# Performance work log

Measured on AMD Instinct MI355X. Metric: run time of the kernel, lower is better.

The kernel has to match this reference:

```python
import jax, jax.numpy as jnp
import numpy as np
import math

N_EMB = 768
N_HEAD = 12
N_INNER = 3072
B, T = 2, 2048
EPS = 1e-4


def _gelu_tanh(x):
    return x * 0.5 * (1.0 + jnp.tanh(math.sqrt(2.0 / math.pi) * (x + 0.044715 * x ** 3)))


def _layernorm(x, scale, bias):
    mean = jnp.mean(x, axis=-1, keepdims=True)
    var = jnp.var(x, axis=-1, keepdims=True, ddof=1)  # torch.var default: unbiased
    return scale * ((x - mean) / jnp.sqrt(var + EPS)) + bias


def setup_inputs() -> dict:
    key = jax.random.key(0)
    ks = jax.random.split(key, 16)
    s_attn = 1.0 / math.sqrt(N_EMB)
    s_mlp1 = 1.0 / math.sqrt(N_EMB)
    s_mlp2 = 1.0 / math.sqrt(N_INNER)
    return {
        "x": jax.random.normal(ks[0], (B, T, N_EMB), dtype=jnp.float32),
        "Wq": jax.random.normal(ks[1], (N_EMB, N_EMB), dtype=jnp.float32) * s_attn,
        "bq": jnp.zeros((N_EMB,), jnp.float32),
        "Wk": jax.random.normal(ks[2], (N_EMB, N_EMB), dtype=jnp.float32) * s_attn,
        "bk": jnp.zeros((N_EMB,), jnp.float32),
        "Wv": jax.random.normal(ks[3], (N_EMB, N_EMB), dtype=jnp.float32) * s_attn,
        "bv": jnp.zeros((N_EMB,), jnp.float32),
        "Wo": jax.random.normal(ks[4], (N_EMB, N_EMB), dtype=jnp.float32) * s_attn,
        "bo": jnp.zeros((N_EMB,), jnp.float32),
        "ln1_s": jnp.ones((N_EMB,), jnp.float32),
        "ln1_b": jnp.zeros((N_EMB,), jnp.float32),
        "W1": jax.random.normal(ks[5], (N_EMB, N_INNER), dtype=jnp.float32) * s_mlp1,
        "b1": jnp.zeros((N_INNER,), jnp.float32),
        "W2": jax.random.normal(ks[6], (N_INNER, N_EMB), dtype=jnp.float32) * s_mlp2,
        "b2": jnp.zeros((N_EMB,), jnp.float32),
        "ln2_s": jnp.ones((N_EMB,), jnp.float32),
        "ln2_b": jnp.zeros((N_EMB,), jnp.float32),
    }


def reference(x, Wq, bq, Wk, bk, Wv, bv, Wo, bo, ln1_s, ln1_b, W1, b1, W2, b2, ln2_s, ln2_b):
    Bx, Tx, C = x.shape
    dh = C // N_HEAD
    # QKV projections -> [B, H, T, dh]
    def split_heads(y):
        return y.reshape(Bx, Tx, N_HEAD, dh).transpose(0, 2, 1, 3)
    q = split_heads(x @ Wq + bq)
    k = split_heads(x @ Wk + bk)
    v = split_heads(x @ Wv + bv)
    # naive full-score causal attention (materializes [B,H,T,T])
    scores = jnp.einsum("bhqd,bhkd->bhqk", q, k)
    causal = jnp.tril(jnp.ones((Tx, Tx), dtype=bool))
    scores = jnp.where(causal, scores, -jnp.inf)
    attn = jax.nn.softmax(scores / math.sqrt(dh), axis=-1)
    ctx = jnp.einsum("bhqk,bhkd->bhqd", attn, v)
    ctx = ctx.transpose(0, 2, 1, 3).reshape(Bx, Tx, C)
    attn_out = ctx @ Wo + bo
    # post-norm residual
    h = _layernorm(x + attn_out, ln1_s, ln1_b)
    mlp_out = _gelu_tanh(h @ W1 + b1) @ W2 + b2
    return _layernorm(h + mlp_out, ln2_s, ln2_b)
```

## Files before the change

kernel.cpp:

```cpp
#include <hip/hip_runtime.h>
#include <math.h>

#define TB  2
#define TT  2048
#define TC  768
#define TH  12
#define TDH 64
#define TI  3072
#define TM  (TB*TT)

typedef __attribute__((ext_vector_type(8))) __bf16 bf16x8;
typedef __attribute__((ext_vector_type(4))) __bf16 bf16x4;
typedef __attribute__((ext_vector_type(4))) float  f32x4;

__device__ __forceinline__ float gelu_tanh(float x) {
    float x3 = x * x * x;
    return 0.5f * x * (1.0f + tanhf(0.7978845608028654f * (x + 0.044715f * x3)));
}

__device__ __forceinline__ void gld_lds16(const void* g, void* l) {
    __builtin_amdgcn_global_load_lds(
        (const __attribute__((address_space(1))) unsigned int*)g,
        (__attribute__((address_space(3))) unsigned int*)l,
        16, 0, 0);
}

#define BK 32

template<int BM_, int BN_, int WM_, int WN_>
__global__ __launch_bounds__(256)
void gemm_mfma(const __bf16* __restrict__ A, const __bf16* __restrict__ Bt,
               const float* __restrict__ b0, const float* __restrict__ b1,
               const float* __restrict__ b2, const float* __restrict__ resid,
               float* __restrict__ outf, __bf16* __restrict__ outb,
               int N, int K, size_t wt_stride, size_t out_stride, int ep)
{
    constexpr int WAVES_N = BN_ / WN_;
    constexpr int TMt = WM_ / 16, TNt = WN_ / 16;
    constexpr int AISS = BM_ / 64, BISS = BN_ / 64;
    constexpr int TILE = (BM_ + BN_) * BK;
    __shared__ __align__(16) __bf16 lds[2 * TILE];

    const int tid  = threadIdx.x;
    const int wave = tid >> 6, lane = tid & 63;
    const int wm = wave / WAVES_N, wn = wave % WAVES_N;
    const int m0 = blockIdx.y * BM_, n0 = blockIdx.x * BN_;
    const int z  = blockIdx.z;

    const __bf16* Bz = Bt + (size_t)z * wt_stride;
    const size_t Kb = (size_t)K * 2;
    const char* Ag = (const char*)A + (size_t)m0 * Kb;
    const char* Bg = (const char*)Bz + (size_t)n0 * Kb;
    const int srow = tid >> 2;
    const int scol = ((tid & 3) ^ ((tid >> 4) & 3)) * 16;
    const int wbase = wave * 1024;

    f32x4 acc[TMt][TNt];
    #pragma unroll
    for (int i = 0; i < TMt; ++i)
        #pragma unroll
        for (int j = 0; j < TNt; ++j)
            acc[i][j] = (f32x4){0.f, 0.f, 0.f, 0.f};

    const int arow = wm * WM_ + (lane & 15);
    const int brow = wn * WN_ + (lane & 15);
    const int koff = (((lane >> 4) ^ ((lane >> 2) & 3))) * 8;

    const int nIter = K / BK;

    auto stage = [&](int buf, int k0b) {
        char* base = (char*)lds + (size_t)buf * TILE * 2;
        #pragma unroll
        for (int s = 0; s < AISS; ++s)
            gld_lds16(Ag + (size_t)(srow + 64 * s) * Kb + k0b + scol,
                      base + s * 4096 + wbase);
        char* bbase = base + BM_ * BK * 2;
        #pragma unroll
        for (int s = 0; s < BISS; ++s)
            gld_lds16(Bg + (size_t)(srow + 64 * s) * Kb + k0b + scol,
                      bbase + s * 4096 + wbase);
    };

    stage(0, 0);
    int buf = 0;
    for (int it = 0; it < nIter; ++it) {
        __syncthreads();
        if (it + 1 < nIter) stage(buf ^ 1, (it + 1) * (BK * 2));

        const __bf16* As = lds + (size_t)buf * TILE;
        const __bf16* Bs = As + BM_ * BK;
        bf16x8 af[TMt], bfr[TNt];
        #pragma unroll
        for (int ti = 0; ti < TMt; ++ti)
            af[ti] = *(const bf16x8*)&As[(arow + ti * 16) * BK + koff];
        #pragma unroll
        for (int tj = 0; tj < TNt; ++tj)
            bfr[tj] = *(const bf16x8*)&Bs[(brow + tj * 16) * BK + koff];
        #pragma unroll
        for (int ti = 0; ti < TMt; ++ti)
            #pragma unroll
            for (int tj = 0; tj < TNt; ++tj)
                acc[ti][tj] = __builtin_amdgcn_mfma_f32_16x16x32_bf16(
                    af[ti], bfr[tj], acc[ti][tj], 0, 0, 0);
        buf ^= 1;
    }

    const int lrow = m0 + wm * WM_ + ((lane >> 4) << 2);
    const int lcol = n0 + wn * WN_ + (lane & 15);

    if (ep == 0) {
        const float* bias = (z == 0) ? b0 : (z == 1) ? b1 : b2;
        __bf16* outz = outb + (size_t)z * out_stride;
        if (z < 2) {
            #pragma unroll
            for (int tj = 0; tj < TNt; ++tj) {
                int n = lcol + tj * 16;
                float bj = bias[n];
                int h = n >> 6, d = n & 63;
                #pragma unroll
                for (int ti = 0; ti < TMt; ++ti)
                    #pragma unroll
                    for (int r = 0; r < 4; ++r) {
                        int m = lrow + ti * 16 + r;
                        int b = m >> 11, t = m & (TT - 1);
                        outz[((size_t)(b * TH + h) * TT + t) * TDH + d] =
                            (__bf16)(acc[ti][tj][r] + bj);
                    }
            }
        } else {
            #pragma unroll
            for (int tj = 0; tj < TNt; ++tj) {
                int n = lcol + tj * 16;
                float bj = bias[n];
                int h = n >> 6, d = n & 63;
                #pragma unroll
                for (int ti = 0; ti < TMt; ++ti) {
                    int m = lrow + ti * 16;
                    int b = m >> 11, t0 = m & (TT - 1);
                    bf16x4 pk;
                    #pragma unroll
                    for (int r = 0; r < 4; ++r)
                        pk[r] = (__bf16)(acc[ti][tj][r] + bj);
                    *(bf16x4*)(outz + ((size_t)(b * TH + h) * TDH + d) * TT + t0) = pk;
                }
            }
        }
    } else if (ep == 1) {
        #pragma unroll
        for (int tj = 0; tj < TNt; ++tj) {
            int n = lcol + tj * 16;
            float bj = b0[n];
            #pragma unroll
            for (int ti = 0; ti < TMt; ++ti)
                #pragma unroll
                for (int r = 0; r < 4; ++r) {
                    int m = lrow + ti * 16 + r;
                    outf[(size_t)m * N + n] =
                        acc[ti][tj][r] + bj + resid[(size_t)m * N + n];
                }
        }
    } else {
        #pragma unroll
        for (int tj = 0; tj < TNt; ++tj) {
            int n = lcol + tj * 16;
            float bj = b0[n];
            #pragma unroll
            for (int ti = 0; ti < TMt; ++ti)
                #pragma unroll
                for (int r = 0; r < 4; ++r) {
                    int m = lrow + ti * 16 + r;
                    outb[(size_t)m * N + n] = (__bf16)gelu_tanh(acc[ti][tj][r] + bj);
                }
        }
    }
}

__global__ __launch_bounds__(256)
void prep_kernel(const float* __restrict__ x,
                 const float* __restrict__ Wq, const float* __restrict__ Wk,
                 const float* __restrict__ Wv, const float* __restrict__ Wo,
                 const float* __restrict__ W1, const float* __restrict__ W2,
                 __bf16* __restrict__ x_bf, __bf16* __restrict__ WqkvT,
                 __bf16* __restrict__ WoT, __bf16* __restrict__ W1T,
                 __bf16* __restrict__ W2T)
{
    const size_t WSZ = (size_t)TC * TC;
    int bid = blockIdx.x;
    if (bid < 1536) {
        int i = (bid * 256 + threadIdx.x) * 8;
        float4 a = *(const float4*)(x + i);
        float4 b = *(const float4*)(x + i + 4);
        bf16x8 v;
        v[0] = (__bf16)a.x; v[1] = (__bf16)a.y; v[2] = (__bf16)a.z; v[3] = (__bf16)a.w;
        v[4] = (__bf16)b.x; v[5] = (__bf16)b.y; v[6] = (__bf16)b.z; v[7] = (__bf16)b.w;
        *(bf16x8*)(x_bf + i) = v;
        return;
    }
    bid -= 1536;
    const float* src; __bf16* dst; int K, N, tloc;
    if (bid < 2304) {
        int w = bid / 576; tloc = bid - w * 576;
        K = TC; N = TC;
        src = (w == 0) ? Wq : (w == 1) ? Wk : (w == 2) ? Wv : Wo;
        dst = (w < 3) ? (WqkvT + (size_t)w * WSZ) : WoT;
    } else if (bid < 4608) {
        tloc = bid - 2304; K = TC; N = TI; src = W1; dst = W1T;
    } else {
        tloc = bid - 4608; K = TI; N = TC; src = W2; dst = W2T;
    }
    int tiles_x = N >> 5;
    int n0 = (tloc % tiles_x) * 32, k0 = (tloc / tiles_x) * 32;

    __shared__ float tile[32][33];
    const int tx = threadIdx.x & 31, ty = threadIdx.x >> 5;
    #pragma unroll
    for (int i = 0; i < 32; i += 8)
        tile[ty + i][tx] = src[(size_t)(k0 + ty + i) * N + n0 + tx];
    __syncthreads();
    #pragma unroll
    for (int i = 0; i < 32; i += 8)
        dst[(size_t)(n0 + ty + i) * K + k0 + tx] = (__bf16)tile[tx][ty + i];
}

__global__ __launch_bounds__(256)
void ln_kernel(const float* __restrict__ in, const float* __restrict__ gs,
               const float* __restrict__ gb, float* __restrict__ out,
               __bf16* __restrict__ out_bf)
{
    const int row = blockIdx.x, tid = threadIdx.x;
    const float* r = in + (size_t)row * TC;
    float x0 = r[tid], x1 = r[tid + 256], x2 = r[tid + 512];
    float s = x0 + x1 + x2;
    float q = x0 * x0 + x1 * x1 + x2 * x2;
    #pragma unroll
    for (int off = 32; off > 0; off >>= 1) {
        s += __shfl_down(s, off);
        q += __shfl_down(q, off);
    }
    __shared__ float partial[8];
    __shared__ float stats[2];
    int wid = tid >> 6, lane = tid & 63;
    if (lane == 0) { partial[wid] = s; partial[wid + 4] = q; }
    __syncthreads();
    if (tid == 0) {
        float S = partial[0] + partial[1] + partial[2] + partial[3];
        float Q = partial[4] + partial[5] + partial[6] + partial[7];
        float mean = S * (1.0f / (float)TC);
        float var = (Q - (float)TC * mean * mean) * (1.0f / (float)(TC - 1));
        stats[0] = mean;
        stats[1] = rsqrtf(var + 1e-4f);
    }
    __syncthreads();
    float mean = stats[0], rstd = stats[1];
    float* w = out + (size_t)row * TC;
    float y0 = gs[tid]       * ((x0 - mean) * rstd) + gb[tid];
    float y1 = gs[tid + 256] * ((x1 - mean) * rstd) + gb[tid + 256];
    float y2 = gs[tid + 512] * ((x2 - mean) * rstd) + gb[tid + 512];
    w[tid] = y0; w[tid + 256] = y1; w[tid + 512] = y2;
    if (out_bf) {
        __bf16* wb = out_bf + (size_t)row * TC;
        wb[tid] = (__bf16)y0; wb[tid + 256] = (__bf16)y1; wb[tid + 512] = (__bf16)y2;
    }
}

#define AP 72
#define ATT_SCALE 0.18033688011112042f

__global__ __launch_bounds__(256)
void attn_mfma(const __bf16* __restrict__ Q, const __bf16* __restrict__ K,
               const __bf16* __restrict__ Vt, __bf16* __restrict__ ctx)
{
    __shared__ __align__(16) __bf16 Ks[2][64 * 64];
    __shared__ __align__(16) __bf16 Vs[2][64 * 64];
    __shared__ __align__(16) __bf16 Ps[64 * AP];

    const int tid  = threadIdx.x;
    const int wave = tid >> 6, lane = tid & 63;
    const int c = lane & 15, g = lane >> 4;
    const int blk = blockIdx.x;

    const int r8   = tid >> 3;
    const int swz  = ((tid & 7) ^ ((tid >> 3) & 7)) * 16;
    const int ldsw = wave * 1024;

    const int x0 = ((g    ) ^ (c & 7)) * 16;
    const int x1 = ((g + 4) ^ (c & 7)) * 16;

    int jobs[3];
    jobs[0] = blk;
    { int q0 = blk / 24, h0 = blk - (blk / 24) * 24; jobs[1] = (31 - q0) * 24 + h0; }
    jobs[2] = (blk < 248) ? (256 + blk) : (520 + (blk - 248));

    for (int jj = 0; jj < 3; ++jj) {
        const int p  = jobs[jj];
        const int qt = p / 24, bh = p - (p / 24) * 24;
        const int q_glob = qt * 64 + wave * 16 + c;

        const __bf16* Qb = Q + (size_t)bh * TT * TDH;
        const char*   Kg = (const char*)(K  + (size_t)bh * TT * TDH);
        const char*   Vg = (const char*)(Vt + (size_t)bh * TDH * TT);

        bf16x8 qf0 = *(const bf16x8*)(Qb + (size_t)q_glob * TDH + g * 8);
        bf16x8 qf1 = *(const bf16x8*)(Qb + (size_t)q_glob * TDH + 32 + g * 8);

        float m_i = -1e30f, l_i = 0.0f;
        f32x4 acc[4];
        #pragma unroll
        for (int m2 = 0; m2 < 4; ++m2) acc[m2] = (f32x4){0.f, 0.f, 0.f, 0.f};

        auto stage = [&](int buf, int kt) {
            const char* kg = Kg + (size_t)(kt * 64 + r8) * 128 + swz;
            const char* vg = Vg + (size_t)r8 * (TT * 2) + kt * 128 + swz;
            char* kl = (char*)&Ks[buf][0] + ldsw;
            char* vl = (char*)&Vs[buf][0] + ldsw;
            gld_lds16(kg,                  kl);
            gld_lds16(kg + 32 * 128,       kl + 4096);
            gld_lds16(vg,                  vl);
            gld_lds16(vg + 32 * (TT * 2),  vl + 4096);
        };

        stage(0, 0);
        __syncthreads();

        for (int kt = 0; kt <= qt; ++kt) {
            const int cur = kt & 1;
            if (kt < qt) stage(cur ^ 1, kt + 1);

            const char* Kc = (const char*)&Ks[cur][0];
            const char* Vc = (const char*)&Vs[cur][0];

            f32x4 st[4];
            #pragma unroll
            for (int g2 = 0; g2 < 4; ++g2) {
                const int row = (16 * g2 + c) * 128;
                bf16x8 af0 = *(const bf16x8*)(Kc + row + x0);
                bf16x8 af1 = *(const bf16x8*)(Kc + row + x1);
                f32x4 z = (f32x4){0.f, 0.f, 0.f, 0.f};
                z = __builtin_amdgcn_mfma_f32_16x16x32_bf16(af0, qf0, z, 0, 0, 0);
                z = __builtin_amdgcn_mfma_f32_16x16x32_bf16(af1, qf1, z, 0, 0, 0);
                st[g2] = z;
            }

            float sv[4][4];
            float mx = -1e30f;
            if (kt == qt) {
                #pragma unroll
                for (int g2 = 0; g2 < 4; ++g2)
                    #pragma unroll
                    for (int r = 0; r < 4; ++r) {
                        int kcol = kt * 64 + 16 * g2 + 4 * g + r;
                        float v = (kcol > q_glob) ? -1e30f : st[g2][r] * ATT_SCALE;
                        sv[g2][r] = v;
                        mx = fmaxf(mx, v);
                    }
            } else {
                #pragma unroll
                for (int g2 = 0; g2 < 4; ++g2)
                    #pragma unroll
                    for (int r = 0; r < 4; ++r) {
                        float v = st[g2][r] * ATT_SCALE;
                        sv[g2][r] = v;
                        mx = fmaxf(mx, v);
                    }
            }
            mx = fmaxf(mx, __shfl_xor(mx, 16));
            mx = fmaxf(mx, __shfl_xor(mx, 32));
            float nm = fmaxf(m_i, mx);
            float corr = exp2f(m_i - nm);
            float ps = 0.f;
            #pragma unroll
            for (int g2 = 0; g2 < 4; ++g2) {
                bf16x4 pk;
                #pragma unroll
                for (int r = 0; r < 4; ++r) {
                    float pp = exp2f(sv[g2][r] - nm);
                    ps += pp;
                    pk[r] = (__bf16)pp;
                }
                *(bf16x4*)&Ps[(wave * 16 + c) * AP + 16 * g2 + 4 * g] = pk;
            }
            ps += __shfl_xor(ps, 16);
            ps += __shfl_xor(ps, 32);
            l_i = l_i * corr + ps;
            m_i = nm;
            #pragma unroll
            for (int m2 = 0; m2 < 4; ++m2) {
                acc[m2][0] *= corr; acc[m2][1] *= corr;
                acc[m2][2] *= corr; acc[m2][3] *= corr;
            }

            bf16x8 pf0 = *(const bf16x8*)&Ps[(wave * 16 + c) * AP + g * 8];
            bf16x8 pf1 = *(const bf16x8*)&Ps[(wave * 16 + c) * AP + 32 + g * 8];
            #pragma unroll
            for (int m2 = 0; m2 < 4; ++m2) {
                const int vrow = (16 * m2 + c) * 128;
                bf16x8 vf0 = *(const bf16x8*)(Vc + vrow + x0);
                bf16x8 vf1 = *(const bf16x8*)(Vc + vrow + x1);
                acc[m2] = __builtin_amdgcn_mfma_f32_16x16x32_bf16(vf0, pf0, acc[m2], 0, 0, 0);
                acc[m2] = __builtin_amdgcn_mfma_f32_16x16x32_bf16(vf1, pf1, acc[m2], 0, 0, 0);
            }

            __syncthreads();
        }

        const int b = bh / TH, h = bh - b * TH;
        float inv = 1.0f / l_i;
        #pragma unroll
        for (int m2 = 0; m2 < 4; ++m2) {
            bf16x4 o;
            #pragma unroll
            for (int r = 0; r < 4; ++r)
                o[r] = (__bf16)(acc[m2][r] * inv);
            *(bf16x4*)(ctx + ((size_t)b * TT + q_glob) * TC + h * TDH + 16 * m2 + 4 * g) = o;
        }
    }
}

extern "C" void kernel_launch(void* const* d_in, const int* in_sizes, int n_in,
                              void* d_out, int out_size, void* d_ws, size_t ws_size,
                              hipStream_t stream)
{
    const float* x    = (const float*)d_in[0];
    const float* Wq   = (const float*)d_in[1];
    const float* bq   = (const float*)d_in[2];
    const float* Wk   = (const float*)d_in[3];
    const float* bk   = (const float*)d_in[4];
    const float* Wv   = (const float*)d_in[5];
    const float* bv   = (const float*)d_in[6];
    const float* Wo   = (const float*)d_in[7];
    const float* bo   = (const float*)d_in[8];
    const float* ln1s = (const float*)d_in[9];
    const float* ln1b = (const float*)d_in[10];
    const float* W1   = (const float*)d_in[11];
    const float* b1   = (const float*)d_in[12];
    const float* W2   = (const float*)d_in[13];
    const float* b2   = (const float*)d_in[14];
    const float* ln2s = (const float*)d_in[15];
    const float* ln2b = (const float*)d_in[16];
    float* out = (float*)d_out;

    const size_t MC  = (size_t)TM * TC;
    const size_t MCB = MC * 2;
    const size_t WSZ = (size_t)TC * TC;
    const size_t W12 = (size_t)TC * TI;

    char* W = (char*)d_ws;
    __bf16* qkvb  = (__bf16*)W;
    __bf16* x_bf  = (__bf16*)(W + 3 * MCB);
    float*  tmp1  = (float*)W;
    __bf16* u_bf  = (__bf16*)W;
    float*  h_f32 = (float*)(W + 4 * MCB);
    __bf16* ctxh  = (__bf16*)(W + 6 * MCB);
    __bf16* wts   = (__bf16*)(W + 7 * MCB);
    __bf16* WqkvT = wts;
    __bf16* WoT   = WqkvT + 3 * WSZ;
    __bf16* W1T   = WoT + WSZ;
    __bf16* W2T   = W1T + W12;

    dim3 blk(256);

    prep_kernel<<<dim3(1536 + 6912), blk, 0, stream>>>(
        x, Wq, Wk, Wv, Wo, W1, W2, x_bf, WqkvT, WoT, W1T, W2T);

    gemm_mfma<128, 128, 64, 64><<<dim3(TC / 128, TM / 128, 3), blk, 0, stream>>>(
        x_bf, WqkvT, bq, bk, bv, nullptr, nullptr, qkvb, TC, TC, WSZ, MC, 0);

    attn_mfma<<<dim3(256), blk, 0, stream>>>(
        qkvb, qkvb + MC, qkvb + 2 * MC, ctxh);

    gemm_mfma<64, 128, 32, 64><<<dim3(TC / 128, TM / 64, 1), blk, 0, stream>>>(
        ctxh, WoT, bo, nullptr, nullptr, x, tmp1, nullptr, TC, TC, 0, 0, 1);

    ln_kernel<<<dim3(TM), blk, 0, stream>>>(tmp1, ln1s, ln1b, h_f32, ctxh);

    gemm_mfma<128, 128, 64, 64><<<dim3(TI / 128, TM / 128, 1), blk, 0, stream>>>(
        ctxh, W1T, b1, nullptr, nullptr, nullptr, nullptr, u_bf, TI, TC, 0, 0, 2);

    gemm_mfma<64, 128, 32, 64><<<dim3(TC / 128, TM / 64, 1), blk, 0, stream>>>(
        u_bf, W2T, b2, nullptr, nullptr, h_f32, out, nullptr, TC, TI, 0, 0, 1);

    ln_kernel<<<dim3(TM), blk, 0, stream>>>(out, ln2s, ln2b, out, nullptr);
}
```

Baseline: 331.5 us.

## Triple-buffer GEMM LDS pipeline with explicit vmcnt waits and retune tile shapes

```diff
diff --git a/kernel.cpp b/kernel.cpp
--- a/kernel.cpp
+++ b/kernel.cpp
@@ -23,6 +23,17 @@
         (const __attribute__((address_space(1))) unsigned int*)g,
         (__attribute__((address_space(3))) unsigned int*)l,
         16, 0, 0);
+}
+
+template<int N>
+__device__ __forceinline__ void vmcnt_wait() {
+    if constexpr (N == 0)      asm volatile("s_waitcnt vmcnt(0)" ::: "memory");
+    else if constexpr (N == 2) asm volatile("s_waitcnt vmcnt(2)" ::: "memory");
+    else if constexpr (N == 3) asm volatile("s_waitcnt vmcnt(3)" ::: "memory");
+    else if constexpr (N == 4) asm volatile("s_waitcnt vmcnt(4)" ::: "memory");
+    else if constexpr (N == 6) asm volatile("s_waitcnt vmcnt(6)" ::: "memory");
+    else if constexpr (N == 8) asm volatile("s_waitcnt vmcnt(8)" ::: "memory");
+    else static_assert(N == 0, "unsupported vmcnt");
 }
 
 #define BK 32
@@ -38,8 +49,9 @@
     constexpr int WAVES_N = BN_ / WN_;
     constexpr int TMt = WM_ / 16, TNt = WN_ / 16;
     constexpr int AISS = BM_ / 64, BISS = BN_ / 64;
+    constexpr int S    = AISS + BISS;
     constexpr int TILE = (BM_ + BN_) * BK;
-    __shared__ __align__(16) __bf16 lds[2 * TILE];
+    __shared__ __align__(16) __bf16 lds[3 * TILE];
 
     const int tid  = threadIdx.x;
     const int wave = tid >> 6, lane = tid & 63;
@@ -68,8 +80,7 @@
 
     const int nIter = K / BK;
 
-    auto stage = [&](int buf, int k0b) {
-        char* base = (char*)lds + (size_t)buf * TILE * 2;
+    auto stage = [&](char* base, int k0b) {
         #pragma unroll
         for (int s = 0; s < AISS; ++s)
             gld_lds16(Ag + (size_t)(srow + 64 * s) * Kb + k0b + scol,
@@ -81,13 +92,26 @@
                       bbase + s * 4096 + wbase);
     };
 
-    stage(0, 0);
-    int buf = 0;
+    char* P0 = (char*)lds;
+    char* P1 = P0 + (size_t)TILE * 2;
+    char* P2 = P1 + (size_t)TILE * 2;
+
+    stage(P0, 0);
+    if (nIter > 1) stage(P1, BK * 2);
+    __builtin_amdgcn_sched_barrier(0);
+    char* cur = P0; char* n1 = P1; char* n2 = P2;
+
     for (int it = 0; it < nIter; ++it) {
-        __syncthreads();
-        if (it + 1 < nIter) stage(buf ^ 1, (it + 1) * (BK * 2));
-
-        const __bf16* As = lds + (size_t)buf * TILE;
+        if (it + 2 < nIter) stage(n2, (it + 2) * (BK * 2));
+        __builtin_amdgcn_sched_barrier(0);
+        const int rem = nIter - 1 - it;
+        if (rem >= 2)      vmcnt_wait<2 * S>();
+        else if (rem == 1) vmcnt_wait<S>();
+        else               vmcnt_wait<0>();
+        __builtin_amdgcn_s_barrier();
+        __builtin_amdgcn_sched_barrier(0);
+
+        const __bf16* As = (const __bf16*)cur;
         const __bf16* Bs = As + BM_ * BK;
         bf16x8 af[TMt], bfr[TNt];
         #pragma unroll
@@ -102,7 +126,10 @@
             for (int tj = 0; tj < TNt; ++tj)
                 acc[ti][tj] = __builtin_amdgcn_mfma_f32_16x16x32_bf16(
                     af[ti], bfr[tj], acc[ti][tj], 0, 0, 0);
-        buf ^= 1;
+
+        __builtin_amdgcn_sched_barrier(0);
+        __builtin_amdgcn_s_barrier();
+        char* t = cur; cur = n1; n1 = n2; n2 = t;
     }
 
     const int lrow = m0 + wm * WM_ + ((lane >> 4) << 2);
@@ -462,13 +489,13 @@
     prep_kernel<<<dim3(1536 + 6912), blk, 0, stream>>>(
         x, Wq, Wk, Wv, Wo, W1, W2, x_bf, WqkvT, WoT, W1T, W2T);
 
-    gemm_mfma<128, 128, 64, 64><<<dim3(TC / 128, TM / 128, 3), blk, 0, stream>>>(
+    gemm_mfma<64, 128, 32, 64><<<dim3(TC / 128, TM / 64, 3), blk, 0, stream>>>(
         x_bf, WqkvT, bq, bk, bv, nullptr, nullptr, qkvb, TC, TC, WSZ, MC, 0);
 
     attn_mfma<<<dim3(256), blk, 0, stream>>>(
         qkvb, qkvb + MC, qkvb + 2 * MC, ctxh);
 
-    gemm_mfma<64, 128, 32, 64><<<dim3(TC / 128, TM / 64, 1), blk, 0, stream>>>(
+    gemm_mfma<64, 64, 32, 32><<<dim3(TC / 64, TM / 64, 1), blk, 0, stream>>>(
         ctxh, WoT, bo, nullptr, nullptr, x, tmp1, nullptr, TC, TC, 0, 0, 1);
 
     ln_kernel<<<dim3(TM), blk, 0, stream>>>(tmp1, ln1s, ln1b, h_f32, ctxh);
@@ -476,7 +503,7 @@
     gemm_mfma<128, 128, 64, 64><<<dim3(TI / 128, TM / 128, 1), blk, 0, stream>>>(
         ctxh, W1T, b1, nullptr, nullptr, nullptr, nullptr, u_bf, TI, TC, 0, 0, 2);
 
-    gemm_mfma<64, 128, 32, 64><<<dim3(TC / 128, TM / 64, 1), blk, 0, stream>>>(
+    gemm_mfma<64, 64, 32, 32><<<dim3(TC / 64, TM / 64, 1), blk, 0, stream>>>(
         u_bf, W2T, b2, nullptr, nullptr, h_f32, out, nullptr, TC, TI, 0, 0, 1);
 
     ln_kernel<<<dim3(TM), blk, 0, stream>>>(out, ln2s, ln2b, out, nullptr);
```

Result: no change. 332.0 us (+0.1%).
